# Kernel tuning notes

Hardware: AMD Instinct MI355X
Metric: run time of the kernel (lower is better)

Reference implementation:

```python
import jax, jax.numpy as jnp
import numpy as np

CH = 256
C8 = CH // 8


def setup_inputs() -> dict:
    key = jax.random.key(0)
    ks = jax.random.split(key, 8)
    scale = 1.0 / np.sqrt(CH)
    x = jax.random.normal(ks[0], (8, CH, 64, 64), dtype=jnp.float32)
    Wq = jax.random.normal(ks[1], (C8, CH), dtype=jnp.float32) * scale
    bq = jnp.zeros((C8,), dtype=jnp.float32)
    Wk = jax.random.normal(ks[2], (C8, CH), dtype=jnp.float32) * scale
    bk = jnp.zeros((C8,), dtype=jnp.float32)
    Wv = jax.random.normal(ks[3], (CH, CH), dtype=jnp.float32) * scale
    bv = jnp.zeros((CH,), dtype=jnp.float32)
    gamma = jnp.full((1,), 0.1, dtype=jnp.float32)  # nonzero so output depends on attention path
    return {"x": x, "Wq": Wq, "bq": bq, "Wk": Wk, "bk": bk, "Wv": Wv, "bv": bv, "gamma": gamma}


def reference(x, Wq, bq, Wk, bk, Wv, bv, gamma):
    b, c, h, w = x.shape
    hw = h * w
    xf = x.reshape(b, c, hw)  # flatten spatial; 1x1 conv == channel matmul
    q = jnp.einsum('oc,bcn->bno', Wq, xf) + bq          # (b, hw, c/8)
    k = jnp.einsum('oc,bcn->bon', Wk, xf) + bk[None, :, None]  # (b, c/8, hw)
    v = jnp.einsum('oc,bcn->bon', Wv, xf) + bv[None, :, None]  # (b, c, hw)
    attn = jax.nn.softmax(jnp.einsum('bno,bom->bnm', q, k), axis=-1)  # (b, hw, hw)
    out = jnp.einsum('bcm,bnm->bcn', v, attn).reshape(b, c, h, w)
    return x + gamma * out
```

## Files before the change

kernel.cpp:

```cpp
#include <hip/hip_runtime.h>
#include <stdint.h>

constexpr int CHN = 256;
constexpr int HW  = 4096;

typedef float f32x4   __attribute__((ext_vector_type(4)));
typedef float f32x16  __attribute__((ext_vector_type(16)));
typedef short bf16x8  __attribute__((ext_vector_type(8)));
typedef short s16x4   __attribute__((ext_vector_type(4)));
typedef uint32_t u32x4 __attribute__((ext_vector_type(4)));

static __device__ __forceinline__ short f2bf(float f) {
  uint32_t u = __builtin_bit_cast(uint32_t, f);
  u += 0x7FFFu + ((u >> 16) & 1u);
  return (short)(u >> 16);
}

static __device__ __forceinline__ uint32_t pkbf(float a, float b) {
  uint32_t r;
  asm("v_cvt_pk_bf16_f32 %0, %1, %2" : "=v"(r) : "v"(a), "v"(b));
  return r;
}

static __device__ __forceinline__ void gl16(const void* g, void* l) {
  __builtin_amdgcn_global_load_lds(
      (const __attribute__((address_space(1))) uint32_t*)g,
      (__attribute__((address_space(3))) uint32_t*)l, 16, 0, 0);
}

__global__ __launch_bounds__(256) void prep_kernel(
    const float* __restrict__ Wq, const float* __restrict__ Wk, const float* __restrict__ Wv,
    const float* __restrict__ bq, const float* __restrict__ bk, const float* __restrict__ bv,
    short* __restrict__ Wb, float* __restrict__ bcat) {
  int idx = blockIdx.x * 256 + threadIdx.x;
  if (idx < 320 * 256) {
    int r = idx >> 8, c = idx & 255;
    float w = (r < 256) ? Wv[idx]
            : (r < 288) ? Wq[(r - 256) * 256 + c]
                        : Wk[(r - 288) * 256 + c];
    Wb[idx] = f2bf(w);
  }
  if (idx < 320)
    bcat[idx] = (idx < 256) ? bv[idx] : (idx < 288) ? bq[idx - 256] : bk[idx - 288];
}

__global__ __launch_bounds__(320) void proj_kernel(
    const float* __restrict__ x, const short* __restrict__ Wb, const float* __restrict__ bcat,
    short* __restrict__ qw, short* __restrict__ kw, short* __restrict__ vws) {
  const int t    = threadIdx.x;
  const int b    = blockIdx.y;
  const int n0   = blockIdx.x * 64;
  const int lane = t & 63;
  const int w    = t >> 6;
  const int ln   = lane & 15;
  const int gp   = lane >> 4;

  const float* xb  = x + (size_t)b * CHN * HW + n0;
  const short* wbp = Wb + (w * 64 + ln) * 256 + gp * 8;

  const f32x4 zv = {0.f, 0.f, 0.f, 0.f};
  f32x4 acc[4][4];
#pragma unroll
  for (int i = 0; i < 4; ++i)
#pragma unroll
    for (int j = 0; j < 4; ++j) acc[i][j] = zv;

#pragma unroll 2
  for (int ks = 0; ks < 8; ++ks) {
    const int k0 = ks * 32;
    bf16x8 a[4];
#pragma unroll
    for (int i = 0; i < 4; ++i)
      a[i] = *(const bf16x8*)(wbp + i * 16 * 256 + k0);
    bf16x8 bxv[4];
#pragma unroll
    for (int j = 0; j < 4; ++j) {
      const float* xc = xb + (size_t)(k0 + gp * 8) * HW + 16 * j + ln;
#pragma unroll
      for (int e = 0; e < 8; ++e) bxv[j][e] = f2bf(xc[(size_t)e * HW]);
    }
#pragma unroll
    for (int i = 0; i < 4; ++i)
#pragma unroll
      for (int j = 0; j < 4; ++j)
        acc[i][j] = __builtin_amdgcn_mfma_f32_16x16x32_bf16(a[i], bxv[j], acc[i][j], 0, 0, 0);
  }

  if (w < 4) {
    short* vblob = vws + ((size_t)(b * 64 + blockIdx.x)) * 16384;
    const int ph = 8 * ((ln >> 2) & 1) + 4 * (ln >> 3) + (ln & 3);
#pragma unroll
    for (int i = 0; i < 4; ++i) {
#pragma unroll
      for (int r = 0; r < 4; ++r) {
        const int c = w * 64 + 16 * i + 4 * gp + r;
        const float bias = bcat[c];
        const int sw = (c & 7) << 3;
#pragma unroll
        for (int j = 0; j < 4; ++j)
          vblob[c * 64 + ((16 * j + ph) ^ sw)] = f2bf(acc[i][j][r] + bias);
      }
    }
  } else {
    constexpr float LOG2E = 1.44269504088896340736f;
#pragma unroll
    for (int j = 0; j < 4; ++j) {
      const size_t nrow = ((size_t)b * HW + n0 + 16 * j + ln) * 32;
#pragma unroll
      for (int i = 0; i < 2; ++i) {
        s16x4 pq, pk;
#pragma unroll
        for (int r = 0; r < 4; ++r) {
          pq[r] = f2bf((acc[i][j][r] + bcat[256 + 16 * i + 4 * gp + r]) * LOG2E);
          pk[r] = f2bf(acc[i + 2][j][r] + bcat[288 + 16 * i + 4 * gp + r]);
        }
        *(s16x4*)(qw + nrow + 16 * i + 4 * gp) = pq;
        *(s16x4*)(kw + nrow + 16 * i + 4 * gp) = pk;
      }
    }
  }
}

__global__ __launch_bounds__(256, 1) void attn_kernel(
    const float* __restrict__ x, const float* __restrict__ gamma,
    const short* __restrict__ qw, const short* __restrict__ kw,
    const short* __restrict__ vws, float* __restrict__ out) {
  __shared__ alignas(16) char sm[2 * 32768];

  const int tid  = threadIdx.x;
  const int lane = tid & 63;
  const int wv   = tid >> 6;
  const int l5   = lane & 31;
  const int h    = lane >> 5;
  const int b    = blockIdx.x & 7;
  const int qt   = blockIdx.x >> 3;
  const int qbase = qt * 128;

  const short* qb    = qw + (size_t)b * HW * 32;
  const short* kb    = kw + (size_t)b * HW * 32;
  const char*  vblob = (const char*)vws + (size_t)b * 64 * 32768;

  const short* qrow = qb + (size_t)(qbase + wv * 32 + l5) * 32 + h * 8;
  const bf16x8 qf0 = *(const bf16x8*)(qrow);
  const bf16x8 qf1 = *(const bf16x8*)(qrow + 16);

  f32x16 z16;
#pragma unroll
  for (int r = 0; r < 16; ++r) z16[r] = 0.f;
  f32x16 O[8];
#pragma unroll
  for (int ct = 0; ct < 8; ++ct) O[ct] = z16;

  float mrun = -1e30f, lrun = 0.f;

  {
    const char* gs = vblob + (wv * 8) * 1024 + lane * 16;
    char* ld = sm + (wv * 8) * 1024;
#pragma unroll
    for (int j = 0; j < 8; ++j) gl16(gs + j * 1024, ld + j * 1024);
  }

  const short* kfb = kb + (size_t)l5 * 32 + h * 8;
  bf16x8 kf00 = *(const bf16x8*)(kfb);
  bf16x8 kf01 = *(const bf16x8*)(kfb + 16);
  bf16x8 kf10 = *(const bf16x8*)(kfb + 1024);
  bf16x8 kf11 = *(const bf16x8*)(kfb + 1024 + 16);

  const int swv = (l5 & 7) << 4;

  for (int it = 0; it < 64; ++it) {
    __syncthreads();
    const char* buf = sm + (it & 1) * 32768;
    if (it < 63) {
      const char* gs = vblob + (size_t)(it + 1) * 32768 + (wv * 8) * 1024 + lane * 16;
      char* ld = sm + ((it + 1) & 1) * 32768 + (wv * 8) * 1024;
#pragma unroll
      for (int j = 0; j < 8; ++j) gl16(gs + j * 1024, ld + j * 1024);
    }

    f32x16 s0 = __builtin_amdgcn_mfma_f32_32x32x16_bf16(kf00, qf0, z16, 0, 0, 0);
    s0 = __builtin_amdgcn_mfma_f32_32x32x16_bf16(kf01, qf1, s0, 0, 0, 0);
    f32x16 s1 = __builtin_amdgcn_mfma_f32_32x32x16_bf16(kf10, qf0, z16, 0, 0, 0);
    s1 = __builtin_amdgcn_mfma_f32_32x32x16_bf16(kf11, qf1, s1, 0, 0, 0);

    if (it < 63) {
      const short* kn = kfb + (size_t)(it + 1) * 2048;
      kf00 = *(const bf16x8*)(kn);
      kf01 = *(const bf16x8*)(kn + 16);
      kf10 = *(const bf16x8*)(kn + 1024);
      kf11 = *(const bf16x8*)(kn + 1024 + 16);
    }

    float tmax = -1e30f;
#pragma unroll
    for (int r = 0; r < 16; ++r) tmax = fmaxf(tmax, fmaxf(s0[r], s1[r]));
    tmax = fmaxf(tmax, __shfl_xor(tmax, 32));
    if (__any(tmax > mrun + 8.f)) {
      const float mnew = fmaxf(mrun, tmax);
      const float al = __builtin_amdgcn_exp2f(mrun - mnew);
      lrun *= al;
      mrun = mnew;
#pragma unroll
      for (int r = 0; r < 16; ++r) {
        const float ar = __shfl(al, (r & 3) + ((r >> 2) << 3) + (h << 2));
#pragma unroll
        for (int ct = 0; ct < 8; ++ct) O[ct][r] *= ar;
      }
    }
    float ps = 0.f;
#pragma unroll
    for (int r = 0; r < 16; ++r) {
      s0[r] = __builtin_amdgcn_exp2f(s0[r] - mrun);
      s1[r] = __builtin_amdgcn_exp2f(s1[r] - mrun);
      ps += s0[r] + s1[r];
    }
    ps += __shfl_xor(ps, 32);
    lrun += ps;

    const char* vb0 = buf + l5 * 128;
#pragma unroll
    for (int mt = 0; mt < 4; ++mt) {
      const int r0 = (mt & 1) * 8;
      uint32_t w0, w1, w2, w3;
      if (mt < 2) {
        w0 = pkbf(s0[r0 + 0], s0[r0 + 1]); w1 = pkbf(s0[r0 + 2], s0[r0 + 3]);
        w2 = pkbf(s0[r0 + 4], s0[r0 + 5]); w3 = pkbf(s0[r0 + 6], s0[r0 + 7]);
      } else {
        w0 = pkbf(s1[r0 + 0], s1[r0 + 1]); w1 = pkbf(s1[r0 + 2], s1[r0 + 3]);
        w2 = pkbf(s1[r0 + 4], s1[r0 + 5]); w3 = pkbf(s1[r0 + 6], s1[r0 + 7]);
      }
      const u32x4 paw = {w0, w1, w2, w3};
      const bf16x8 pa = __builtin_bit_cast(bf16x8, paw);
      const char* vbm = vb0 + ((32 * mt + 16 * h) ^ swv);
#pragma unroll
      for (int ct = 0; ct < 8; ++ct) {
        const bf16x8 vf = *(const bf16x8*)(vbm + ct * 4096);
        O[ct] = __builtin_amdgcn_mfma_f32_32x32x16_bf16(pa, vf, O[ct], 0, 0, 0);
      }
    }
  }

  const float g0 = gamma[0];
  float linv[16];
#pragma unroll
  for (int r = 0; r < 16; ++r)
    linv[r] = g0 / __shfl(lrun, (r & 3) + ((r >> 2) << 3) + (h << 2));

  float* eo = (float*)sm;
  for (int ct = 0; ct < 8; ++ct) {
    __syncthreads();
#pragma unroll
    for (int r = 0; r < 16; ++r)
      eo[l5 * 132 + wv * 32 + ((r & 3) + ((r >> 2) << 3) + (h << 2))] = O[ct][r] * linv[r];
    __syncthreads();
    const int cl = tid >> 3, seg = tid & 7;
    const size_t gi = ((size_t)b * CHN + ct * 32 + cl) * HW + qbase + seg * 16;
#pragma unroll
    for (int u = 0; u < 4; ++u) {
      const f32x4 xv = *(const f32x4*)(x + gi + u * 4);
      const f32x4 ov = *(const f32x4*)(&eo[cl * 132 + seg * 16 + u * 4]);
      *(f32x4*)(out + gi + u * 4) = xv + ov;
    }
  }
}

extern "C" void kernel_launch(void* const* d_in, const int* in_sizes, int n_in,
                              void* d_out, int out_size, void* d_ws, size_t ws_size,
                              hipStream_t stream) {
  const float* x     = (const float*)d_in[0];
  const float* Wq    = (const float*)d_in[1];
  const float* bq    = (const float*)d_in[2];
  const float* Wk    = (const float*)d_in[3];
  const float* bk    = (const float*)d_in[4];
  const float* Wv    = (const float*)d_in[5];
  const float* bv    = (const float*)d_in[6];
  const float* gamma = (const float*)d_in[7];
  float* out = (float*)d_out;

  char* ws = (char*)d_ws;
  short* qw   = (short*)(ws);
  short* kw   = (short*)(ws + (2u << 20));
  short* vws  = (short*)(ws + (4u << 20));
  short* Wb   = (short*)(ws + (20u << 20));
  float* bcat = (float*)(ws + (20u << 20) + (256u << 10));

  prep_kernel<<<320, 256, 0, stream>>>(Wq, Wk, Wv, bq, bk, bv, Wb, bcat);
  proj_kernel<<<dim3(64, 8), 320, 0, stream>>>(x, Wb, bcat, qw, kw, vws);
  attn_kernel<<<256, 256, 0, stream>>>(x, gamma, qw, kw, vws, out);
}
```

Baseline: 153.7 us.

## Switch P·V matmul to FP8 with padded V layout and finer barrier waits

```diff
diff --git a/kernel.cpp b/kernel.cpp
--- a/kernel.cpp
+++ b/kernel.cpp
@@ -3,12 +3,15 @@
 
 constexpr int CHN = 256;
 constexpr int HW  = 4096;
+
+constexpr int VROW  = 72;
+constexpr int VTILE = 256 * VROW;
+constexpr int VBATCH = 64 * VTILE;
 
 typedef float f32x4   __attribute__((ext_vector_type(4)));
 typedef float f32x16  __attribute__((ext_vector_type(16)));
 typedef short bf16x8  __attribute__((ext_vector_type(8)));
 typedef short s16x4   __attribute__((ext_vector_type(4)));
-typedef uint32_t u32x4 __attribute__((ext_vector_type(4)));
 
 static __device__ __forceinline__ short f2bf(float f) {
   uint32_t u = __builtin_bit_cast(uint32_t, f);
@@ -16,10 +19,8 @@
   return (short)(u >> 16);
 }
 
-static __device__ __forceinline__ uint32_t pkbf(float a, float b) {
-  uint32_t r;
-  asm("v_cvt_pk_bf16_f32 %0, %1, %2" : "=v"(r) : "v"(a), "v"(b));
-  return r;
+static __device__ __forceinline__ uint8_t f2fp8(float f) {
+  return (uint8_t)__builtin_amdgcn_cvt_pk_fp8_f32(f, f, 0, false);
 }
 
 static __device__ __forceinline__ void gl16(const void* g, void* l) {
@@ -46,7 +47,7 @@
 
 __global__ __launch_bounds__(320) void proj_kernel(
     const float* __restrict__ x, const short* __restrict__ Wb, const float* __restrict__ bcat,
-    short* __restrict__ qw, short* __restrict__ kw, short* __restrict__ vws) {
+    short* __restrict__ qw, short* __restrict__ kw, uint8_t* __restrict__ v8) {
   const int t    = threadIdx.x;
   const int b    = blockIdx.y;
   const int n0   = blockIdx.x * 64;
@@ -87,18 +88,17 @@
   }
 
   if (w < 4) {
-    short* vblob = vws + ((size_t)(b * 64 + blockIdx.x)) * 16384;
-    const int ph = 8 * ((ln >> 2) & 1) + 4 * (ln >> 3) + (ln & 3);
+    uint8_t* vblob = v8 + ((size_t)(b * 64 + blockIdx.x)) * VTILE;
+    const int phi = 8 * ((ln >> 2) & 1) + 4 * (ln >> 3) + (ln & 3);
 #pragma unroll
     for (int i = 0; i < 4; ++i) {
 #pragma unroll
       for (int r = 0; r < 4; ++r) {
         const int c = w * 64 + 16 * i + 4 * gp + r;
         const float bias = bcat[c];
-        const int sw = (c & 7) << 3;
 #pragma unroll
         for (int j = 0; j < 4; ++j)
-          vblob[c * 64 + ((16 * j + ph) ^ sw)] = f2bf(acc[i][j][r] + bias);
+          vblob[c * VROW + 16 * j + phi] = f2fp8(acc[i][j][r] + bias);
       }
     }
   } else {
@@ -124,8 +124,8 @@
 __global__ __launch_bounds__(256, 1) void attn_kernel(
     const float* __restrict__ x, const float* __restrict__ gamma,
     const short* __restrict__ qw, const short* __restrict__ kw,
-    const short* __restrict__ vws, float* __restrict__ out) {
-  __shared__ alignas(16) char sm[2 * 32768];
+    const uint8_t* __restrict__ v8, float* __restrict__ out) {
+  __shared__ alignas(16) char sm[2 * VTILE];
 
   const int tid  = threadIdx.x;
   const int lane = tid & 63;
@@ -136,9 +136,9 @@
   const int qt   = blockIdx.x >> 3;
   const int qbase = qt * 128;
 
-  const short* qb    = qw + (size_t)b * HW * 32;
-  const short* kb    = kw + (size_t)b * HW * 32;
-  const char*  vblob = (const char*)vws + (size_t)b * 64 * 32768;
+  const short*   qb    = qw + (size_t)b * HW * 32;
+  const short*   kb    = kw + (size_t)b * HW * 32;
+  const uint8_t* vblob = v8 + (size_t)b * VBATCH;
 
   const short* qrow = qb + (size_t)(qbase + wv * 32 + l5) * 32 + h * 8;
   const bf16x8 qf0 = *(const bf16x8*)(qrow);
@@ -150,33 +150,34 @@
   f32x16 O[8];
 #pragma unroll
   for (int ct = 0; ct < 8; ++ct) O[ct] = z16;
-
   float mrun = -1e30f, lrun = 0.f;
 
-  {
-    const char* gs = vblob + (wv * 8) * 1024 + lane * 16;
-    char* ld = sm + (wv * 8) * 1024;
-#pragma unroll
-    for (int j = 0; j < 8; ++j) gl16(gs + j * 1024, ld + j * 1024);
-  }
-
+  auto stage = [&](int tile, char* lbuf) {
+    const uint8_t* gt = vblob + (size_t)tile * VTILE;
+#pragma unroll
+    for (int j = 0; j < 5; ++j) {
+      const int cidx = wv + 4 * j;
+      if (cidx < 18)
+        gl16(gt + cidx * 1024 + lane * 16, lbuf + cidx * 1024);
+    }
+  };
+
+  stage(0, sm);
+  asm volatile("" ::: "memory");
   const short* kfb = kb + (size_t)l5 * 32 + h * 8;
   bf16x8 kf00 = *(const bf16x8*)(kfb);
   bf16x8 kf01 = *(const bf16x8*)(kfb + 16);
   bf16x8 kf10 = *(const bf16x8*)(kfb + 1024);
   bf16x8 kf11 = *(const bf16x8*)(kfb + 1024 + 16);
 
-  const int swv = (l5 & 7) << 4;
-
   for (int it = 0; it < 64; ++it) {
-    __syncthreads();
-    const char* buf = sm + (it & 1) * 32768;
-    if (it < 63) {
-      const char* gs = vblob + (size_t)(it + 1) * 32768 + (wv * 8) * 1024 + lane * 16;
-      char* ld = sm + ((it + 1) & 1) * 32768 + (wv * 8) * 1024;
-#pragma unroll
-      for (int j = 0; j < 8; ++j) gl16(gs + j * 1024, ld + j * 1024);
-    }
+    asm volatile("s_waitcnt vmcnt(4)" ::: "memory");
+    __builtin_amdgcn_s_barrier();
+    asm volatile("" ::: "memory");
+
+    const char* buf = sm + (it & 1) * VTILE;
+    if (it < 63) stage(it + 1, sm + ((it + 1) & 1) * VTILE);
+    asm volatile("" ::: "memory");
 
     f32x16 s0 = __builtin_amdgcn_mfma_f32_32x32x16_bf16(kf00, qf0, z16, 0, 0, 0);
     s0 = __builtin_amdgcn_mfma_f32_32x32x16_bf16(kf01, qf1, s0, 0, 0, 0);
@@ -202,7 +203,7 @@
       mrun = mnew;
 #pragma unroll
       for (int r = 0; r < 16; ++r) {
-        const float ar = __shfl(al, (r & 3) + ((r >> 2) << 3) + (h << 2));
+        const float ar = __shfl(al, (r & 3) + 8 * (r >> 2) + 4 * h);
 #pragma unroll
         for (int ct = 0; ct < 8; ++ct) O[ct][r] *= ar;
       }
@@ -217,25 +218,28 @@
     ps += __shfl_xor(ps, 32);
     lrun += ps;
 
-    const char* vb0 = buf + l5 * 128;
+    const char* vbl = buf + l5 * VROW;
 #pragma unroll
     for (int mt = 0; mt < 4; ++mt) {
       const int r0 = (mt & 1) * 8;
-      uint32_t w0, w1, w2, w3;
+      int lo, hi;
       if (mt < 2) {
-        w0 = pkbf(s0[r0 + 0], s0[r0 + 1]); w1 = pkbf(s0[r0 + 2], s0[r0 + 3]);
-        w2 = pkbf(s0[r0 + 4], s0[r0 + 5]); w3 = pkbf(s0[r0 + 6], s0[r0 + 7]);
+        lo = __builtin_amdgcn_cvt_pk_fp8_f32(s0[r0 + 0], s0[r0 + 1], 0,  false);
+        lo = __builtin_amdgcn_cvt_pk_fp8_f32(s0[r0 + 2], s0[r0 + 3], lo, true);
+        hi = __builtin_amdgcn_cvt_pk_fp8_f32(s0[r0 + 4], s0[r0 + 5], 0,  false);
+        hi = __builtin_amdgcn_cvt_pk_fp8_f32(s0[r0 + 6], s0[r0 + 7], hi, true);
       } else {
-        w0 = pkbf(s1[r0 + 0], s1[r0 + 1]); w1 = pkbf(s1[r0 + 2], s1[r0 + 3]);
-        w2 = pkbf(s1[r0 + 4], s1[r0 + 5]); w3 = pkbf(s1[r0 + 6], s1[r0 + 7]);
-      }
-      const u32x4 paw = {w0, w1, w2, w3};
-      const bf16x8 pa = __builtin_bit_cast(bf16x8, paw);
-      const char* vbm = vb0 + ((32 * mt + 16 * h) ^ swv);
+        lo = __builtin_amdgcn_cvt_pk_fp8_f32(s1[r0 + 0], s1[r0 + 1], 0,  false);
+        lo = __builtin_amdgcn_cvt_pk_fp8_f32(s1[r0 + 2], s1[r0 + 3], lo, true);
+        hi = __builtin_amdgcn_cvt_pk_fp8_f32(s1[r0 + 4], s1[r0 + 5], 0,  false);
+        hi = __builtin_amdgcn_cvt_pk_fp8_f32(s1[r0 + 6], s1[r0 + 7], hi, true);
+      }
+      const long long pa = (long long)(((uint64_t)(uint32_t)hi << 32) | (uint32_t)lo);
+      const int vo = 16 * mt + 8 * h;
 #pragma unroll
       for (int ct = 0; ct < 8; ++ct) {
-        const bf16x8 vf = *(const bf16x8*)(vbm + ct * 4096);
-        O[ct] = __builtin_amdgcn_mfma_f32_32x32x16_bf16(pa, vf, O[ct], 0, 0, 0);
+        const long long vf = *(const long long*)(vbl + ct * (32 * VROW) + vo);
+        O[ct] = __builtin_amdgcn_mfma_f32_32x32x16_fp8_fp8(pa, vf, O[ct], 0, 0, 0);
       }
     }
   }
@@ -244,14 +248,14 @@
   float linv[16];
 #pragma unroll
   for (int r = 0; r < 16; ++r)
-    linv[r] = g0 / __shfl(lrun, (r & 3) + ((r >> 2) << 3) + (h << 2));
+    linv[r] = g0 / __shfl(lrun, (r & 3) + 8 * (r >> 2) + 4 * h);
 
   float* eo = (float*)sm;
   for (int ct = 0; ct < 8; ++ct) {
     __syncthreads();
 #pragma unroll
     for (int r = 0; r < 16; ++r)
-      eo[l5 * 132 + wv * 32 + ((r & 3) + ((r >> 2) << 3) + (h << 2))] = O[ct][r] * linv[r];
+      eo[l5 * 132 + wv * 32 + ((r & 3) + 8 * (r >> 2) + 4 * h)] = O[ct][r] * linv[r];
     __syncthreads();
     const int cl = tid >> 3, seg = tid & 7;
     const size_t gi = ((size_t)b * CHN + ct * 32 + cl) * HW + qbase + seg * 16;
@@ -278,13 +282,13 @@
   float* out = (float*)d_out;
 
   char* ws = (char*)d_ws;
-  short* qw   = (short*)(ws);
-  short* kw   = (short*)(ws + (2u << 20));
-  short* vws  = (short*)(ws + (4u << 20));
-  short* Wb   = (short*)(ws + (20u << 20));
-  float* bcat = (float*)(ws + (20u << 20) + (256u << 10));
+  short*   qw   = (short*)(ws);
+  short*   kw   = (short*)(ws + (2u << 20));
+  uint8_t* v8   = (uint8_t*)(ws + (4u << 20));
+  short*   Wb   = (short*)(ws + (20u << 20));
+  float*   bcat = (float*)(ws + (20u << 20) + (256u << 10));
 
   prep_kernel<<<320, 256, 0, stream>>>(Wq, Wk, Wv, bq, bk, bv, Wb, bcat);
-  proj_kernel<<<dim3(64, 8), 320, 0, stream>>>(x, Wb, bcat, qw, kw, vws);
-  attn_kernel<<<256, 256, 0, stream>>>(x, gamma, qw, kw, vws, out);
-}
+  proj_kernel<<<dim3(64, 8), 320, 0, stream>>>(x, Wb, bcat, qw, kw, v8);
+  attn_kernel<<<256, 256, 0, stream>>>(x, gamma, qw, kw, v8, out);
+}
```

Result: slower. 159.8 us (median of 4 runs) (+3.9%).
